# Kernel tuning notes

Measured on AMD Instinct MI355X. Metric: run time of the kernel, lower is better.

Reference implementation:

```python
import jax, jax.numpy as jnp
import numpy as np

B, I, O, E = 1024, 512, 512, 16


def setup_inputs() -> dict:
    key = jax.random.key(0)
    k_x, k_c, k_w = jax.random.split(key, 3)
    x = jax.random.normal(k_x, (B, I), dtype=jnp.float32)
    coeffs = jax.random.uniform(k_c, (B, E), dtype=jnp.float32)
    expert_weights = jax.random.normal(k_w, (E, I, O), dtype=jnp.float32) * 0.01
    expert_biases = jnp.zeros((E, O), dtype=jnp.float32)
    return {"x": x, "coeffs": coeffs, "expert_weights": expert_weights, "expert_biases": expert_biases}


def reference(x, coeffs, expert_weights, expert_biases):
    # Soft-MoE: per-sample convex blend of expert linear layers.
    # Equivalent to out[b] = x[b] @ (sum_e coeffs[b,e] * W[e]) + sum_e coeffs[b,e] * b[e]
    # Contract x with each expert first (avoids the [B,I,O] combined-weight tensor).
    per_expert = jnp.einsum('bi,eio->beo', x, expert_weights)   # [B,E,O]
    out = jnp.einsum('be,beo->bo', coeffs, per_expert)          # [B,O]
    out = out + coeffs @ expert_biases                          # [B,O]
    return out
```

## Files before the change

### kernel.cpp

```cpp
#include <hip/hip_runtime.h>

#define B_  1024
#define I_  512
#define O_  512
#define E_  16
#define K_  8192

#define KSPLIT 16
#define KRANGE (K_ / KSPLIT)
#define BK 64
#define NSTEP (KRANGE / BK)
#define NTILE 32

typedef __attribute__((ext_vector_type(8))) short short8;
typedef __attribute__((ext_vector_type(8))) unsigned short ushort8;
typedef __attribute__((ext_vector_type(4))) unsigned short ushort4v;
typedef __attribute__((ext_vector_type(4))) float f32x4;

__device__ __forceinline__ unsigned short f2bf(float f) {
  union { float f; unsigned u; } v; v.f = f;
  unsigned r = v.u + 0x7fffu + ((v.u >> 16) & 1u);
  return (unsigned short)(r >> 16);
}
__device__ __forceinline__ float bf2f(unsigned short h) {
  union { unsigned u; float f; } v; v.u = ((unsigned)h) << 16;
  return v.f;
}

__device__ __forceinline__ void gload_lds16(const unsigned short* g, unsigned short* l) {
  __builtin_amdgcn_global_load_lds(
      (const __attribute__((address_space(1))) void*)g,
      (__attribute__((address_space(3))) void*)l, 16, 0, 0);
}

__global__ void prep_kernel(const float* __restrict__ x,
                            const float* __restrict__ coeffs,
                            const float* __restrict__ W,
                            unsigned short* __restrict__ A,
                            unsigned short* __restrict__ Wt) {
  __shared__ unsigned short tile[64][65];
  if (blockIdx.x < 4096) {
    int t = blockIdx.x * 256 + threadIdx.x;
    int base = t * 8;
    int b = base >> 13;
    int rem = base & (K_ - 1);
    int e = rem >> 9;
    int i0 = rem & (I_ - 1);
    float c = coeffs[b * E_ + e];
    const float4* xp = (const float4*)(x + b * I_ + i0);
    float4 v0 = xp[0], v1 = xp[1];
    ushort8 r;
    r[0] = f2bf(v0.x * c); r[1] = f2bf(v0.y * c);
    r[2] = f2bf(v0.z * c); r[3] = f2bf(v0.w * c);
    r[4] = f2bf(v1.x * c); r[5] = f2bf(v1.y * c);
    r[6] = f2bf(v1.z * c); r[7] = f2bf(v1.w * c);
    *(ushort8*)(A + base) = r;
  } else {
    int bw = blockIdx.x - 4096;
    int kt = (bw & 127) << 6;
    int nt = (bw >> 7) << 6;
    int t = threadIdx.x;
#pragma unroll
    for (int it = 0; it < 16; ++it) {
      int idx = it * 256 + t;
      int r = idx >> 6, c = idx & 63;
      tile[r][c] = f2bf(W[(long)(kt + r) * O_ + nt + c]);
    }
    __syncthreads();
#pragma unroll
    for (int it = 0; it < 2; ++it) {
      int idx = it * 256 + t;
      int r2 = idx >> 3;
      int c2 = (idx & 7) * 8;
      ushort8 v;
#pragma unroll
      for (int j = 0; j < 8; ++j) v[j] = tile[c2 + j][r2];
      *(ushort8*)(Wt + (long)(nt + r2) * K_ + kt + c2) = v;
    }
  }
}

__global__ void bias_init_kernel(const float* __restrict__ coeffs,
                                 const float* __restrict__ eb,
                                 float* __restrict__ out) {
  int t = blockIdx.x * 256 + threadIdx.x;
  int b = t >> 7;
  int o4 = (t & 127) * 4;
  const float* cb = coeffs + b * E_;
  float4 acc = {0.f, 0.f, 0.f, 0.f};
#pragma unroll
  for (int e = 0; e < E_; ++e) {
    float c = cb[e];
    float4 bv = *(const float4*)(eb + e * O_ + o4);
    acc.x += c * bv.x; acc.y += c * bv.y; acc.z += c * bv.z; acc.w += c * bv.w;
  }
  *(float4*)(out + b * O_ + o4) = acc;
}

template <int USE_PART>
__global__ __launch_bounds__(256) void gemm_kernel(
    const unsigned short* __restrict__ A,
    const unsigned short* __restrict__ Wt,
    float* __restrict__ out,
    unsigned short* __restrict__ part) {
  __shared__ unsigned short As[2][128 * 64];
  __shared__ unsigned short Bs[2][128 * 64];
  int bx = blockIdx.x;
  int ks = bx & (KSPLIT - 1);
  int tile = bx >> 4;
  int tm = tile >> 2, tn = tile & 3;
  int brow = tm * 128, bcol = tn * 128;
  long k0 = (long)ks * KRANGE;

  int tid = threadIdx.x;
  int lane = tid & 63, wave = tid >> 6;
  int wr = wave >> 1, wc = wave & 1;

  f32x4 acc[4][4];
#pragma unroll
  for (int m = 0; m < 4; ++m)
#pragma unroll
    for (int n = 0; n < 4; ++n) acc[m][n] = (f32x4){0.f, 0.f, 0.f, 0.f};

  int lr8 = lane >> 3;
  int jj = lane & 7;
  int ksrc = (jj ^ lr8) * 8;
  const unsigned short* gA = A + (long)(brow + lr8) * K_ + k0 + ksrc;
  const unsigned short* gB = Wt + (long)(bcol + lr8) * K_ + k0 + ksrc;

  auto STAGE = [&](int buf, int s) {
    long kof = (long)s * BK;
#pragma unroll
    for (int i = 0; i < 4; ++i) {
      int chunk = i * 4 + wave;
      gload_lds16(gA + (long)chunk * 8 * K_ + kof, &As[buf][chunk * 512]);
      gload_lds16(gB + (long)chunk * 8 * K_ + kof, &Bs[buf][chunk * 512]);
    }
  };

  auto COMPUTE = [&](int buf) {
#pragma unroll
    for (int kk = 0; kk < 2; ++kk) {
      int kbyte = kk * 64 + (lane >> 4) * 16;
      short8 af[4], bfr[4];
#pragma unroll
      for (int m = 0; m < 4; ++m) {
        int r = wr * 64 + m * 16 + (lane & 15);
        int off = r * 64 + ((kbyte ^ ((r & 7) << 4)) >> 1);
        af[m] = *(const short8*)(&As[buf][off]);
      }
#pragma unroll
      for (int n = 0; n < 4; ++n) {
        int r = wc * 64 + n * 16 + (lane & 15);
        int off = r * 64 + ((kbyte ^ ((r & 7) << 4)) >> 1);
        bfr[n] = *(const short8*)(&Bs[buf][off]);
      }
#pragma unroll
      for (int m = 0; m < 4; ++m)
#pragma unroll
        for (int n = 0; n < 4; ++n)
          acc[m][n] = __builtin_amdgcn_mfma_f32_16x16x32_bf16(af[m], bfr[n], acc[m][n], 0, 0, 0);
    }
  };

  STAGE(0, 0);
  __syncthreads();
#pragma unroll
  for (int s = 0; s < NSTEP; ++s) {
    if (s + 1 < NSTEP) STAGE((s + 1) & 1, s + 1);
    COMPUTE(s & 1);
    __syncthreads();
  }

  int crow = wr * 64 + (lane >> 4) * 4;
  int ccol = wc * 64 + (lane & 15);
  if (USE_PART) {
    unsigned short* pb = part + (long)ks * B_ * O_;
#pragma unroll
    for (int m = 0; m < 4; ++m)
#pragma unroll
      for (int n = 0; n < 4; ++n) {
        long rbase = (long)(brow + crow + m * 16) * O_ + bcol + ccol + n * 16;
#pragma unroll
        for (int j = 0; j < 4; ++j)
          pb[rbase + (long)j * O_] = f2bf(acc[m][n][j]);
      }
  } else {
#pragma unroll
    for (int m = 0; m < 4; ++m)
#pragma unroll
      for (int n = 0; n < 4; ++n) {
        float* p = out + (long)(brow + crow + m * 16) * O_ + bcol + ccol + n * 16;
#pragma unroll
        for (int j = 0; j < 4; ++j)
          atomicAdd(p + (long)j * O_, acc[m][n][j]);
      }
  }
}

__global__ void reduce_bias_kernel(const unsigned short* __restrict__ part,
                                   const float* __restrict__ coeffs,
                                   const float* __restrict__ eb,
                                   float* __restrict__ out) {
  int t = blockIdx.x * 256 + threadIdx.x;
  int b = t >> 7;
  int o4 = (t & 127) * 4;
  float4 acc = {0.f, 0.f, 0.f, 0.f};
#pragma unroll
  for (int ksl = 0; ksl < KSPLIT; ++ksl) {
    ushort4v v = *(const ushort4v*)(part + (long)ksl * B_ * O_ + (long)b * O_ + o4);
    acc.x += bf2f(v[0]); acc.y += bf2f(v[1]);
    acc.z += bf2f(v[2]); acc.w += bf2f(v[3]);
  }
  const float* cb = coeffs + b * E_;
#pragma unroll
  for (int e = 0; e < E_; ++e) {
    float c = cb[e];
    float4 bv = *(const float4*)(eb + e * O_ + o4);
    acc.x += c * bv.x; acc.y += c * bv.y; acc.z += c * bv.z; acc.w += c * bv.w;
  }
  *(float4*)(out + (long)b * O_ + o4) = acc;
}

extern "C" void kernel_launch(void* const* d_in, const int* in_sizes, int n_in,
                              void* d_out, int out_size, void* d_ws, size_t ws_size,
                              hipStream_t stream) {
  const float* x      = (const float*)d_in[0];
  const float* coeffs = (const float*)d_in[1];
  const float* W      = (const float*)d_in[2];
  const float* eb     = (const float*)d_in[3];
  float* out = (float*)d_out;

  size_t A_bytes  = (size_t)B_ * K_ * 2;
  size_t Wt_bytes = (size_t)O_ * K_ * 2;
  size_t part_bytes = (size_t)KSPLIT * B_ * O_ * 2;
  unsigned short* A    = (unsigned short*)d_ws;
  unsigned short* Wt   = (unsigned short*)((char*)d_ws + A_bytes);
  unsigned short* part = (unsigned short*)((char*)d_ws + A_bytes + Wt_bytes);
  bool use_part = ws_size >= A_bytes + Wt_bytes + part_bytes;

  prep_kernel<<<dim3(4096 + 1024), 256, 0, stream>>>(x, coeffs, W, A, Wt);
  if (use_part) {
    gemm_kernel<1><<<dim3(NTILE * KSPLIT), 256, 0, stream>>>(A, Wt, out, part);
    reduce_bias_kernel<<<dim3(B_ * O_ / 4 / 256), 256, 0, stream>>>(part, coeffs, eb, out);
  } else {
    bias_init_kernel<<<dim3(B_ * O_ / 4 / 256), 256, 0, stream>>>(coeffs, eb, out);
    gemm_kernel<0><<<dim3(NTILE * KSPLIT), 256, 0, stream>>>(A, Wt, out, part);
  }
}
```

Before: 34.05 us.

## Compute per-expert GEMMs on unscaled x and apply coefficients in combine

Stops materializing the coeff-scaled activation matrix A of shape [B, E*I] in bf16 and converts only x to bf16. Each workgroup computes one expert's x@W[e] tile, and the split dimension changes from K-slices to experts. The combine kernel then weights each expert's partial by coeffs and adds the bias. This removes the large A write and read in prep and the GEMM, and adds a blockIdx swizzle so workgroups that share x tiles are grouped. A trade-off is that partials are now rounded to bf16 before the coefficient is applied.

```diff
diff --git a/kernel.cpp b/kernel.cpp
--- a/kernel.cpp
+++ b/kernel.cpp
@@ -6,11 +6,9 @@
 #define E_  16
 #define K_  8192
 
-#define KSPLIT 16
-#define KRANGE (K_ / KSPLIT)
 #define BK 64
-#define NSTEP (KRANGE / BK)
-#define NTILE 32
+#define NSTEP (I_ / BK)
+#define NWG  (E_ * (B_ / 128) * (O_ / 128))
 
 typedef __attribute__((ext_vector_type(8))) short short8;
 typedef __attribute__((ext_vector_type(8))) unsigned short ushort8;
@@ -34,29 +32,20 @@
 }
 
 __global__ void prep_kernel(const float* __restrict__ x,
-                            const float* __restrict__ coeffs,
                             const float* __restrict__ W,
-                            unsigned short* __restrict__ A,
+                            unsigned short* __restrict__ xb,
                             unsigned short* __restrict__ Wt) {
   __shared__ unsigned short tile[64][65];
-  if (blockIdx.x < 4096) {
-    int t = blockIdx.x * 256 + threadIdx.x;
-    int base = t * 8;
-    int b = base >> 13;
-    int rem = base & (K_ - 1);
-    int e = rem >> 9;
-    int i0 = rem & (I_ - 1);
-    float c = coeffs[b * E_ + e];
-    const float4* xp = (const float4*)(x + b * I_ + i0);
+  if (blockIdx.x < 256) {
+    int base = (blockIdx.x * 256 + threadIdx.x) * 8;
+    const float4* xp = (const float4*)(x + base);
     float4 v0 = xp[0], v1 = xp[1];
     ushort8 r;
-    r[0] = f2bf(v0.x * c); r[1] = f2bf(v0.y * c);
-    r[2] = f2bf(v0.z * c); r[3] = f2bf(v0.w * c);
-    r[4] = f2bf(v1.x * c); r[5] = f2bf(v1.y * c);
-    r[6] = f2bf(v1.z * c); r[7] = f2bf(v1.w * c);
-    *(ushort8*)(A + base) = r;
+    r[0] = f2bf(v0.x); r[1] = f2bf(v0.y); r[2] = f2bf(v0.z); r[3] = f2bf(v0.w);
+    r[4] = f2bf(v1.x); r[5] = f2bf(v1.y); r[6] = f2bf(v1.z); r[7] = f2bf(v1.w);
+    *(ushort8*)(xb + base) = r;
   } else {
-    int bw = blockIdx.x - 4096;
+    int bw = blockIdx.x - 256;
     int kt = (bw & 127) << 6;
     int nt = (bw >> 7) << 6;
     int t = threadIdx.x;
@@ -99,18 +88,19 @@
 
 template <int USE_PART>
 __global__ __launch_bounds__(256) void gemm_kernel(
-    const unsigned short* __restrict__ A,
+    const unsigned short* __restrict__ xb,
     const unsigned short* __restrict__ Wt,
+    const float* __restrict__ coeffs,
     float* __restrict__ out,
     unsigned short* __restrict__ part) {
   __shared__ unsigned short As[2][128 * 64];
   __shared__ unsigned short Bs[2][128 * 64];
   int bx = blockIdx.x;
-  int ks = bx & (KSPLIT - 1);
-  int tile = bx >> 4;
+  int swz = (bx & 7) * (NWG / 8) + (bx >> 3);
+  int e = swz >> 5;
+  int tile = swz & 31;
   int tm = tile >> 2, tn = tile & 3;
   int brow = tm * 128, bcol = tn * 128;
-  long k0 = (long)ks * KRANGE;
 
   int tid = threadIdx.x;
   int lane = tid & 63, wave = tid >> 6;
@@ -125,15 +115,15 @@
   int lr8 = lane >> 3;
   int jj = lane & 7;
   int ksrc = (jj ^ lr8) * 8;
-  const unsigned short* gA = A + (long)(brow + lr8) * K_ + k0 + ksrc;
-  const unsigned short* gB = Wt + (long)(bcol + lr8) * K_ + k0 + ksrc;
+  const unsigned short* gA = xb + (long)(brow + lr8) * I_ + ksrc;
+  const unsigned short* gB = Wt + (long)(bcol + lr8) * K_ + e * I_ + ksrc;
 
   auto STAGE = [&](int buf, int s) {
     long kof = (long)s * BK;
 #pragma unroll
     for (int i = 0; i < 4; ++i) {
       int chunk = i * 4 + wave;
-      gload_lds16(gA + (long)chunk * 8 * K_ + kof, &As[buf][chunk * 512]);
+      gload_lds16(gA + (long)chunk * 8 * I_ + kof, &As[buf][chunk * 512]);
       gload_lds16(gB + (long)chunk * 8 * K_ + kof, &Bs[buf][chunk * 512]);
     }
   };
@@ -175,7 +165,7 @@
   int crow = wr * 64 + (lane >> 4) * 4;
   int ccol = wc * 64 + (lane & 15);
   if (USE_PART) {
-    unsigned short* pb = part + (long)ks * B_ * O_;
+    unsigned short* pb = part + (long)e * B_ * O_;
 #pragma unroll
     for (int m = 0; m < 4; ++m)
 #pragma unroll
@@ -190,32 +180,31 @@
     for (int m = 0; m < 4; ++m)
 #pragma unroll
       for (int n = 0; n < 4; ++n) {
-        float* p = out + (long)(brow + crow + m * 16) * O_ + bcol + ccol + n * 16;
-#pragma unroll
-        for (int j = 0; j < 4; ++j)
-          atomicAdd(p + (long)j * O_, acc[m][n][j]);
-      }
-  }
-}
-
-__global__ void reduce_bias_kernel(const unsigned short* __restrict__ part,
-                                   const float* __restrict__ coeffs,
-                                   const float* __restrict__ eb,
-                                   float* __restrict__ out) {
+#pragma unroll
+        for (int j = 0; j < 4; ++j) {
+          int row = brow + crow + m * 16 + j;
+          float c = coeffs[row * E_ + e];
+          atomicAdd(out + (long)row * O_ + bcol + ccol + n * 16, c * acc[m][n][j]);
+        }
+      }
+  }
+}
+
+__global__ void combine_kernel(const unsigned short* __restrict__ part,
+                               const float* __restrict__ coeffs,
+                               const float* __restrict__ eb,
+                               float* __restrict__ out) {
   int t = blockIdx.x * 256 + threadIdx.x;
   int b = t >> 7;
   int o4 = (t & 127) * 4;
+  const float* cb = coeffs + b * E_;
   float4 acc = {0.f, 0.f, 0.f, 0.f};
-#pragma unroll
-  for (int ksl = 0; ksl < KSPLIT; ++ksl) {
-    ushort4v v = *(const ushort4v*)(part + (long)ksl * B_ * O_ + (long)b * O_ + o4);
-    acc.x += bf2f(v[0]); acc.y += bf2f(v[1]);
-    acc.z += bf2f(v[2]); acc.w += bf2f(v[3]);
-  }
-  const float* cb = coeffs + b * E_;
 #pragma unroll
   for (int e = 0; e < E_; ++e) {
     float c = cb[e];
+    ushort4v v = *(const ushort4v*)(part + (long)e * B_ * O_ + (long)b * O_ + o4);
+    acc.x += c * bf2f(v[0]); acc.y += c * bf2f(v[1]);
+    acc.z += c * bf2f(v[2]); acc.w += c * bf2f(v[3]);
     float4 bv = *(const float4*)(eb + e * O_ + o4);
     acc.x += c * bv.x; acc.y += c * bv.y; acc.z += c * bv.z; acc.w += c * bv.w;
   }
@@ -231,20 +220,20 @@
   const float* eb     = (const float*)d_in[3];
   float* out = (float*)d_out;
 
-  size_t A_bytes  = (size_t)B_ * K_ * 2;
-  size_t Wt_bytes = (size_t)O_ * K_ * 2;
-  size_t part_bytes = (size_t)KSPLIT * B_ * O_ * 2;
-  unsigned short* A    = (unsigned short*)d_ws;
-  unsigned short* Wt   = (unsigned short*)((char*)d_ws + A_bytes);
-  unsigned short* part = (unsigned short*)((char*)d_ws + A_bytes + Wt_bytes);
-  bool use_part = ws_size >= A_bytes + Wt_bytes + part_bytes;
-
-  prep_kernel<<<dim3(4096 + 1024), 256, 0, stream>>>(x, coeffs, W, A, Wt);
+  size_t xb_bytes   = (size_t)B_ * I_ * 2;
+  size_t Wt_bytes   = (size_t)O_ * K_ * 2;
+  size_t part_bytes = (size_t)E_ * B_ * O_ * 2;
+  unsigned short* xb   = (unsigned short*)d_ws;
+  unsigned short* Wt   = (unsigned short*)((char*)d_ws + xb_bytes);
+  unsigned short* part = (unsigned short*)((char*)d_ws + xb_bytes + Wt_bytes);
+  bool use_part = ws_size >= xb_bytes + Wt_bytes + part_bytes;
+
+  prep_kernel<<<dim3(256 + 1024), 256, 0, stream>>>(x, W, xb, Wt);
   if (use_part) {
-    gemm_kernel<1><<<dim3(NTILE * KSPLIT), 256, 0, stream>>>(A, Wt, out, part);
-    reduce_bias_kernel<<<dim3(B_ * O_ / 4 / 256), 256, 0, stream>>>(part, coeffs, eb, out);
+    gemm_kernel<1><<<dim3(NWG), 256, 0, stream>>>(xb, Wt, coeffs, out, part);
+    combine_kernel<<<dim3(B_ * O_ / 4 / 256), 256, 0, stream>>>(part, coeffs, eb, out);
   } else {
     bias_init_kernel<<<dim3(B_ * O_ / 4 / 256), 256, 0, stream>>>(coeffs, eb, out);
-    gemm_kernel<0><<<dim3(NTILE * KSPLIT), 256, 0, stream>>>(A, Wt, out, part);
-  }
-}
+    gemm_kernel<0><<<dim3(NWG), 256, 0, stream>>>(xb, Wt, coeffs, out, part);
+  }
+}
```

Measured after the change: 30.18 us, median of 3. -11.4%, faster.
